# Kernel tuning notes

Measured on AMD Instinct MI355X. Metric: run time of the kernel, lower is better.

## Reference

```python
import jax, jax.numpy as jnp
import numpy as np

EMBED_DIM = 1024
NUM_HEADS = 16
HEAD_DIM = EMBED_DIM // NUM_HEADS


def setup_inputs() -> dict:
    key = jax.random.key(0)
    ks = jax.random.split(key, 9)
    B, S, E = 4, 2048, EMBED_DIM
    scale = 1.0 / np.sqrt(E)
    x = jax.random.normal(ks[0], (B, S, E), dtype=jnp.float32)
    # Linear layers: weight [E, E] (out, in) and bias [E], torch-style init scale
    Wq = jax.random.uniform(ks[1], (E, E), jnp.float32, -scale, scale)
    bq = jax.random.uniform(ks[2], (E,), jnp.float32, -scale, scale)
    Wk = jax.random.uniform(ks[3], (E, E), jnp.float32, -scale, scale)
    bk = jax.random.uniform(ks[4], (E,), jnp.float32, -scale, scale)
    Wv = jax.random.uniform(ks[5], (E, E), jnp.float32, -scale, scale)
    bv = jax.random.uniform(ks[6], (E,), jnp.float32, -scale, scale)
    Wo = jax.random.uniform(ks[7], (E, E), jnp.float32, -scale, scale)
    bo = jax.random.uniform(ks[8], (E,), jnp.float32, -scale, scale)
    return {"x": x, "Wq": Wq, "bq": bq, "Wk": Wk, "bk": bk,
            "Wv": Wv, "bv": bv, "Wo": Wo, "bo": bo}


def reference(x, Wq, bq, Wk, bk, Wv, bv, Wo, bo):
    B, S, E = x.shape
    H, D = NUM_HEADS, HEAD_DIM

    def proj(W, b):
        # torch Linear: x @ W.T + b ; reshape to [B, H, S, D]
        y = jnp.einsum('bse,fe->bsf', x, W) + b
        return y.reshape(B, S, H, D).transpose(0, 2, 1, 3)

    Q = proj(Wq, bq)
    K = proj(Wk, bk)
    V = proj(Wv, bv)
    scores = jnp.einsum('bhqd,bhkd->bhqk', Q, K) / jnp.sqrt(
        jnp.asarray(D, dtype=jnp.float32))
    attn = jax.nn.softmax(scores, axis=-1)
    out = jnp.einsum('bhqk,bhkd->bhqd', attn, V)
    out = out.transpose(0, 2, 1, 3).reshape(B, S, E)
    out = jnp.einsum('bse,fe->bsf', out, Wo) + bo
    return out
```

## Files before the change

### kernel.cpp

```cpp
#include <hip/hip_runtime.h>
#include <math.h>

#define SEQ 2048
#define EMB 1024
#define NH 16
#define HD 64
#define BATCH 4
#define MROWS (BATCH * SEQ)

typedef unsigned short u16;
typedef unsigned int u32;
typedef _Float16 f16;
using half8   = __attribute__((ext_vector_type(8))) f16;
using fp16x2  = __attribute__((ext_vector_type(2))) __fp16;
using vfloat4 = __attribute__((ext_vector_type(4))) float;

__device__ __forceinline__ u16 f2h(float f) {
    union { f16 h; u16 u; } x; x.h = (f16)f; return x.u;
}
__device__ __forceinline__ u32 pk2h(float a, float b) {
    union { fp16x2 h; u32 u; } x;
    x.h = __builtin_amdgcn_cvt_pkrtz(a, b);
    return x.u;
}
__device__ __forceinline__ float exp2v(float x) {
    float r; asm("v_exp_f32 %0, %1" : "=v"(r) : "v"(x)); return r;
}

__device__ __forceinline__ void gload16(const void* g, void* l) {
    __builtin_amdgcn_global_load_lds(
        (const __attribute__((address_space(1))) void*)g,
        (__attribute__((address_space(3))) void*)l, 16, 0, 0);
}

__global__ __launch_bounds__(256) void cvt_kernel(
    const float* __restrict__ in, u16* __restrict__ out, int n4)
{
    int idx = blockIdx.x * 256 + threadIdx.x;
    if (idx >= n4) return;
    float4 v = ((const float4*)in)[idx];
    u32 lo = pk2h(v.x, v.y);
    u32 hi = pk2h(v.z, v.w);
    ((uint2*)out)[idx] = make_uint2(lo, hi);
}

__global__ __launch_bounds__(256) void gemm_qkv_kernel(
    const u16* __restrict__ A, const u16* __restrict__ Wqkv,
    const float* __restrict__ bq, const float* __restrict__ bk,
    const float* __restrict__ bv,
    u16* __restrict__ Qo, u16* __restrict__ Ko, u16* __restrict__ Vo,
    float sq)
{
    __shared__ char lds[16384];
    char* As = lds;
    char* Bs = lds + 8192;
    const int tid = threadIdx.x, wave = tid >> 6, lane = tid & 63;
    const int bm = blockIdx.y, bn = blockIdx.x;
    const int mat = bn >> 3;
    const int wr = wave >> 1, wc = wave & 1;

    const int srow  = wave * 16 + (lane >> 2);
    const int sslot = lane & 3;
    const int ldso  = wave * 1024 + (lane << 4);
    const u16* Ab = A    + (size_t)bm * 128 * EMB;
    const u16* Wb = Wqkv + (size_t)bn * 128 * EMB;

    vfloat4 acc[4][4] = {};

    for (int k0 = 0; k0 < EMB; k0 += 32) {
        __syncthreads();
        #pragma unroll
        for (int i2 = 0; i2 < 2; ++i2) {
            int row = i2 * 64 + srow;
            int ko  = ((sslot ^ ((row >> 1) & 3)) << 3);
            gload16(Ab + (size_t)row * EMB + k0 + ko, As + i2 * 4096 + ldso);
            gload16(Wb + (size_t)row * EMB + k0 + ko, Bs + i2 * 4096 + ldso);
        }
        __syncthreads();

        half8 af[4], bfr[4];
        #pragma unroll
        for (int m = 0; m < 4; ++m) {
            int r = wr * 64 + m * 16 + (lane & 15);
            af[m] = *(const half8*)(As + r * 64 + ((((lane >> 4) ^ ((r >> 1) & 3)) << 4)));
        }
        #pragma unroll
        for (int n = 0; n < 4; ++n) {
            int r = wc * 64 + n * 16 + (lane & 15);
            bfr[n] = *(const half8*)(Bs + r * 64 + ((((lane >> 4) ^ ((r >> 1) & 3)) << 4)));
        }
        #pragma unroll
        for (int m = 0; m < 4; ++m)
            #pragma unroll
            for (int n = 0; n < 4; ++n)
                acc[m][n] = __builtin_amdgcn_mfma_f32_16x16x32_f16(af[m], bfr[n], acc[m][n], 0, 0, 0);
    }

    const float* bp = (mat == 0) ? bq : ((mat == 1) ? bk : bv);
    const float scale = (mat == 0) ? sq : 1.0f;
    u16* Co = (mat == 0) ? Qo : ((mat == 1) ? Ko : Vo);
    const int row0 = bm * 128 + wr * 64;
    const int col0 = (bn & 7) * 128 + wc * 64;

    #pragma unroll
    for (int n = 0; n < 4; ++n) {
        int col = col0 + n * 16 + (lane & 15);
        float bb = bp[col];
        int h = col >> 6, d = col & 63;
        #pragma unroll
        for (int m = 0; m < 4; ++m)
            #pragma unroll
            for (int j = 0; j < 4; ++j) {
                int row = row0 + m * 16 + (lane >> 4) * 4 + j;
                int b = row >> 11, s = row & (SEQ - 1);
                float val = (acc[m][n][j] + bb) * scale;
                if (mat != 2) {
                    Co[(((size_t)(b * NH + h)) * SEQ + s) * HD + d] = f2h(val);
                } else {
                    Co[(((size_t)(b * NH + h)) * HD + d) * SEQ + s] = f2h(val);
                }
            }
    }
}

__global__ __launch_bounds__(256) void gemm_f16_kernel(
    const u16* __restrict__ A, const u16* __restrict__ W,
    const float* __restrict__ bias, float* __restrict__ C)
{
    __shared__ char lds[16384];
    char* As = lds;
    char* Bs = lds + 8192;
    const int tid = threadIdx.x, wave = tid >> 6, lane = tid & 63;
    const int bm = blockIdx.y, bn = blockIdx.x;
    const int wr = wave >> 1, wc = wave & 1;

    const int srow  = wave * 16 + (lane >> 2);
    const int sslot = lane & 3;
    const int ldso  = wave * 1024 + (lane << 4);
    const u16* Ab = A + (size_t)bm * 128 * EMB;
    const u16* Wb = W + (size_t)bn * 128 * EMB;

    vfloat4 acc[4][4] = {};

    for (int k0 = 0; k0 < EMB; k0 += 32) {
        __syncthreads();
        #pragma unroll
        for (int i2 = 0; i2 < 2; ++i2) {
            int row = i2 * 64 + srow;
            int ko  = ((sslot ^ ((row >> 1) & 3)) << 3);
            gload16(Ab + (size_t)row * EMB + k0 + ko, As + i2 * 4096 + ldso);
            gload16(Wb + (size_t)row * EMB + k0 + ko, Bs + i2 * 4096 + ldso);
        }
        __syncthreads();

        half8 af[4], bfr[4];
        #pragma unroll
        for (int m = 0; m < 4; ++m) {
            int r = wr * 64 + m * 16 + (lane & 15);
            af[m] = *(const half8*)(As + r * 64 + ((((lane >> 4) ^ ((r >> 1) & 3)) << 4)));
        }
        #pragma unroll
        for (int n = 0; n < 4; ++n) {
            int r = wc * 64 + n * 16 + (lane & 15);
            bfr[n] = *(const half8*)(Bs + r * 64 + ((((lane >> 4) ^ ((r >> 1) & 3)) << 4)));
        }
        #pragma unroll
        for (int m = 0; m < 4; ++m)
            #pragma unroll
            for (int n = 0; n < 4; ++n)
                acc[m][n] = __builtin_amdgcn_mfma_f32_16x16x32_f16(af[m], bfr[n], acc[m][n], 0, 0, 0);
    }

    const int row0 = bm * 128 + wr * 64, col0 = bn * 128 + wc * 64;
    #pragma unroll
    for (int n = 0; n < 4; ++n) {
        int col = col0 + n * 16 + (lane & 15);
        float bb = bias[col];
        #pragma unroll
        for (int m = 0; m < 4; ++m)
            #pragma unroll
            for (int j = 0; j < 4; ++j) {
                int row = row0 + m * 16 + (lane >> 4) * 4 + j;
                C[(size_t)row * EMB + col] = acc[m][n][j] + bb;
            }
    }
}

__device__ __forceinline__ void stage_rows(const u16* g, int rstride, char* dst,
                                           int wave, int lane) {
    int r = wave * 8 + (lane >> 3), sl = lane & 7;
    #pragma unroll
    for (int i2 = 0; i2 < 2; ++i2) {
        int row = i2 * 32 + r;
        gload16(g + (size_t)row * rstride + ((sl ^ (row & 7)) << 3),
                dst + i2 * 4096 + wave * 1024 + (lane << 4));
    }
}

__global__ __launch_bounds__(256) void attn_kernel(
    const u16* __restrict__ Q, const u16* __restrict__ K,
    const u16* __restrict__ Vt, u16* __restrict__ O)
{
    __shared__ char lds[40960];
    char* QPs = lds;
    char* Kb0 = lds + 8192;
    char* Kb1 = lds + 16384;
    char* Vb0 = lds + 24576;
    char* Vb1 = lds + 32768;

    const int tid = threadIdx.x, wave = tid >> 6, lane = tid & 63;
    const int c = lane >> 4, li = lane & 15;
    const int bh = blockIdx.y;
    const int q0 = blockIdx.x << 6;

    const u16* Qg = Q  + ((size_t)bh * SEQ + q0) * HD;
    const u16* Kg = K  + (size_t)bh * SEQ * HD;
    const u16* Vg = Vt + (size_t)bh * HD * SEQ;

    stage_rows(Qg, HD, QPs, wave, lane);
    stage_rows(Kg, HD, Kb0, wave, lane);
    stage_rows(Vg, SEQ, Vb0, wave, lane);
    __syncthreads();

    half8 qf[2];
    {
        int q = wave * 16 + li;
        #pragma unroll
        for (int cc = 0; cc < 2; ++cc)
            qf[cc] = *(const half8*)(QPs + q * 128 + (((4 * cc + c) ^ (q & 7)) << 4));
    }

    const half8 ones8 = {1, 1, 1, 1, 1, 1, 1, 1};
    char* Pw = QPs + wave * 2048;
    vfloat4 o[4] = {};
    vfloat4 o5 = {};
    float m_ = -1e30f;

    for (int kt = 0; kt < SEQ / 64; ++kt) {
        char* Kc = (kt & 1) ? Kb1 : Kb0;
        char* Vc = (kt & 1) ? Vb1 : Vb0;
        if (kt < SEQ / 64 - 1) {
            stage_rows(Kg + (size_t)(kt + 1) * 64 * HD, HD,
                       (kt & 1) ? Kb0 : Kb1, wave, lane);
            stage_rows(Vg + (kt + 1) * 64, SEQ,
                       (kt & 1) ? Vb0 : Vb1, wave, lane);
        }

        vfloat4 st[4] = {};
        #pragma unroll
        for (int n = 0; n < 4; ++n) {
            int key = 16 * n + li;
            #pragma unroll
            for (int cc = 0; cc < 2; ++cc) {
                half8 kb = *(const half8*)(Kc + key * 128 + (((4 * cc + c) ^ (li & 7)) << 4));
                st[n] = __builtin_amdgcn_mfma_f32_16x16x32_f16(kb, qf[cc], st[n], 0, 0, 0);
            }
        }

        float t0 = fmaxf(fmaxf(st[0][0], st[0][1]), fmaxf(st[0][2], st[0][3]));
        float t1 = fmaxf(fmaxf(st[1][0], st[1][1]), fmaxf(st[1][2], st[1][3]));
        float t2 = fmaxf(fmaxf(st[2][0], st[2][1]), fmaxf(st[2][2], st[2][3]));
        float t3 = fmaxf(fmaxf(st[3][0], st[3][1]), fmaxf(st[3][2], st[3][3]));
        float pm = fmaxf(fmaxf(t0, t1), fmaxf(t2, t3));
        pm = fmaxf(pm, __shfl_xor(pm, 16));
        pm = fmaxf(pm, __shfl_xor(pm, 32));

        if (__any(pm > m_ + 8.0f)) {
            float mn = fmaxf(m_, pm);
            float al = exp2v(m_ - mn);
            m_ = mn;
            o5 = o5 * al;
            #pragma unroll
            for (int n = 0; n < 4; ++n) o[n] = o[n] * al;
        }

        #pragma unroll
        for (int n = 0; n < 4; ++n)
            #pragma unroll
            for (int j = 0; j < 4; ++j)
                st[n][j] = exp2v(st[n][j] - m_);

        #pragma unroll
        for (int n = 0; n < 4; ++n) {
            u32 w0 = pk2h(st[n][0], st[n][1]);
            u32 w1 = pk2h(st[n][2], st[n][3]);
            *(uint2*)(Pw + li * 128 + (((2 * n + (c >> 1)) ^ (li & 7)) << 4) + ((c & 1) << 3))
                = make_uint2(w0, w1);
        }

        half8 pf[2];
        #pragma unroll
        for (int cc = 0; cc < 2; ++cc)
            pf[cc] = *(const half8*)(Pw + li * 128 + (((4 * cc + c) ^ (li & 7)) << 4));

        #pragma unroll
        for (int n = 0; n < 4; ++n) {
            int r = 16 * n + li;
            #pragma unroll
            for (int cc = 0; cc < 2; ++cc) {
                half8 vf = *(const half8*)(Vc + r * 128 + (((4 * cc + c) ^ (li & 7)) << 4));
                o[n] = __builtin_amdgcn_mfma_f32_16x16x32_f16(vf, pf[cc], o[n], 0, 0, 0);
            }
        }
        #pragma unroll
        for (int cc = 0; cc < 2; ++cc)
            o5 = __builtin_amdgcn_mfma_f32_16x16x32_f16(ones8, pf[cc], o5, 0, 0, 0);

        __syncthreads();
    }

    const int b = bh >> 4, h = bh & 15;
    const int sg = q0 + wave * 16 + li;
    const size_t rowo = ((size_t)b * SEQ + sg) * EMB + h * 64;
    float inv = 1.0f / o5[0];
    #pragma unroll
    for (int n = 0; n < 4; ++n) {
        u32 w0 = pk2h(o[n][0] * inv, o[n][1] * inv);
        u32 w1 = pk2h(o[n][2] * inv, o[n][3] * inv);
        *(uint2*)(O + rowo + 16 * n + 4 * c) = make_uint2(w0, w1);
    }
}

extern "C" void kernel_launch(void* const* d_in, const int* in_sizes, int n_in,
                              void* d_out, int out_size, void* d_ws, size_t ws_size,
                              hipStream_t stream) {
    const float* x  = (const float*)d_in[0];
    const float* Wq = (const float*)d_in[1];
    const float* bq = (const float*)d_in[2];
    const float* Wk = (const float*)d_in[3];
    const float* bk = (const float*)d_in[4];
    const float* Wv = (const float*)d_in[5];
    const float* bv = (const float*)d_in[6];
    const float* Wo = (const float*)d_in[7];
    const float* bo = (const float*)d_in[8];
    float* out = (float*)d_out;

    char* ws = (char*)d_ws;
    u16* xh   = (u16*)(ws);
    u16* Qh   = (u16*)(ws + ((size_t)16 << 20));
    u16* Kh   = (u16*)(ws + ((size_t)32 << 20));
    u16* Vh   = (u16*)(ws + ((size_t)48 << 20));
    u16* Ah   = (u16*)(ws + ((size_t)64 << 20));
    u16* Wqkv = (u16*)(ws + ((size_t)80 << 20));
    u16* Woh  = (u16*)(ws + ((size_t)88 << 20));

    const int nX4 = (MROWS * EMB) / 4;
    const int nW4 = (EMB * EMB) / 4;

    cvt_kernel<<<(nX4 + 255) / 256, 256, 0, stream>>>(x, xh, nX4);
    cvt_kernel<<<(nW4 + 255) / 256, 256, 0, stream>>>(Wq, Wqkv, nW4);
    cvt_kernel<<<(nW4 + 255) / 256, 256, 0, stream>>>(Wk, Wqkv + (size_t)EMB * EMB, nW4);
    cvt_kernel<<<(nW4 + 255) / 256, 256, 0, stream>>>(Wv, Wqkv + (size_t)2 * EMB * EMB, nW4);
    cvt_kernel<<<(nW4 + 255) / 256, 256, 0, stream>>>(Wo, Woh, nW4);

    const float SCALE_Q = 0.125f * 1.4426950408889634f;
    gemm_qkv_kernel<<<dim3(3 * EMB / 128, MROWS / 128), 256, 0, stream>>>(
        xh, Wqkv, bq, bk, bv, Qh, Kh, Vh, SCALE_Q);

    attn_kernel<<<dim3(SEQ / 64, BATCH * NH), 256, 0, stream>>>(Qh, Kh, Vh, Ah);

    gemm_f16_kernel<<<dim3(EMB / 128, MROWS / 128), 256, 0, stream>>>(Ah, Woh, bo, out);
}
```

Measured before the change: 265.4 us.

## Process two query tiles per attention block and merge conversion kernels

The attention kernel now handles 128 query rows per block, with each wave keeping two 16-row query fragments. This reuses every staged K/V tile for twice the queries, halving K/V global traffic and the block count. The five fp32-to-fp16 conversion launches are merged into one kernel to cut launch overhead. The cost is higher register pressure and fewer blocks (1024 vs 2048), which may lower occupancy.

```diff
diff --git a/kernel.cpp b/kernel.cpp
--- a/kernel.cpp
+++ b/kernel.cpp
@@ -33,15 +33,27 @@
         (__attribute__((address_space(3))) void*)l, 16, 0, 0);
 }
 
-__global__ __launch_bounds__(256) void cvt_kernel(
-    const float* __restrict__ in, u16* __restrict__ out, int n4)
+__global__ __launch_bounds__(256) void cvt5_kernel(
+    const float* __restrict__ x,  const float* __restrict__ wq,
+    const float* __restrict__ wk, const float* __restrict__ wv,
+    const float* __restrict__ wo,
+    uint2* __restrict__ xh, uint2* __restrict__ wqkv, uint2* __restrict__ woh)
 {
-    int idx = blockIdx.x * 256 + threadIdx.x;
-    if (idx >= n4) return;
-    float4 v = ((const float4*)in)[idx];
-    u32 lo = pk2h(v.x, v.y);
-    u32 hi = pk2h(v.z, v.w);
-    ((uint2*)out)[idx] = make_uint2(lo, hi);
+    int gid = blockIdx.x * 256 + threadIdx.x;
+    const float4* src; uint2* dst; int o;
+    if (gid < (1 << 21)) {
+        src = (const float4*)x; dst = xh; o = gid;
+    } else {
+        int g = gid - (1 << 21);
+        int r = g >> 18;
+        o = g & ((1 << 18) - 1);
+        if      (r == 0) { src = (const float4*)wq; dst = wqkv; }
+        else if (r == 1) { src = (const float4*)wk; dst = wqkv + (1 << 18); }
+        else if (r == 2) { src = (const float4*)wv; dst = wqkv + (2 << 18); }
+        else             { src = (const float4*)wo; dst = woh; }
+    }
+    float4 v = src[o];
+    dst[o] = make_uint2(pk2h(v.x, v.y), pk2h(v.z, v.w));
 }
 
 __global__ __launch_bounds__(256) void gemm_qkv_kernel(
@@ -211,7 +223,7 @@
     const int tid = threadIdx.x, wave = tid >> 6, lane = tid & 63;
     const int c = lane >> 4, li = lane & 15;
     const int bh = blockIdx.y;
-    const int q0 = blockIdx.x << 6;
+    const int q0 = blockIdx.x << 7;
 
     const u16* Qg = Q  + ((size_t)bh * SEQ + q0) * HD;
     const u16* Kg = K  + (size_t)bh * SEQ * HD;
@@ -222,19 +234,23 @@
     stage_rows(Vg, SEQ, Vb0, wave, lane);
     __syncthreads();
 
-    half8 qf[2];
-    {
-        int q = wave * 16 + li;
-        #pragma unroll
-        for (int cc = 0; cc < 2; ++cc)
-            qf[cc] = *(const half8*)(QPs + q * 128 + (((4 * cc + c) ^ (q & 7)) << 4));
-    }
+    half8 qf[2][2];
+    const int q = wave * 16 + li;
+    #pragma unroll
+    for (int cc = 0; cc < 2; ++cc)
+        qf[0][cc] = *(const half8*)(QPs + q * 128 + (((4 * cc + c) ^ (q & 7)) << 4));
+    __syncthreads();
+    stage_rows(Qg + (size_t)64 * HD, HD, QPs, wave, lane);
+    __syncthreads();
+    #pragma unroll
+    for (int cc = 0; cc < 2; ++cc)
+        qf[1][cc] = *(const half8*)(QPs + q * 128 + (((4 * cc + c) ^ (q & 7)) << 4));
 
     const half8 ones8 = {1, 1, 1, 1, 1, 1, 1, 1};
     char* Pw = QPs + wave * 2048;
-    vfloat4 o[4] = {};
-    vfloat4 o5 = {};
-    float m_ = -1e30f;
+    vfloat4 o0[4] = {}, o1[4] = {};
+    vfloat4 l0 = {}, l1 = {};
+    float m0 = -1e30f, m1 = -1e30f;
 
     for (int kt = 0; kt < SEQ / 64; ++kt) {
         char* Kc = (kt & 1) ? Kb1 : Kb0;
@@ -246,52 +262,78 @@
                        (kt & 1) ? Vb0 : Vb1, wave, lane);
         }
 
-        vfloat4 st[4] = {};
+        vfloat4 s0[4] = {}, s1[4] = {};
         #pragma unroll
         for (int n = 0; n < 4; ++n) {
             int key = 16 * n + li;
             #pragma unroll
             for (int cc = 0; cc < 2; ++cc) {
                 half8 kb = *(const half8*)(Kc + key * 128 + (((4 * cc + c) ^ (li & 7)) << 4));
-                st[n] = __builtin_amdgcn_mfma_f32_16x16x32_f16(kb, qf[cc], st[n], 0, 0, 0);
+                s0[n] = __builtin_amdgcn_mfma_f32_16x16x32_f16(kb, qf[0][cc], s0[n], 0, 0, 0);
+                s1[n] = __builtin_amdgcn_mfma_f32_16x16x32_f16(kb, qf[1][cc], s1[n], 0, 0, 0);
             }
         }
 
-        float t0 = fmaxf(fmaxf(st[0][0], st[0][1]), fmaxf(st[0][2], st[0][3]));
-        float t1 = fmaxf(fmaxf(st[1][0], st[1][1]), fmaxf(st[1][2], st[1][3]));
-        float t2 = fmaxf(fmaxf(st[2][0], st[2][1]), fmaxf(st[2][2], st[2][3]));
-        float t3 = fmaxf(fmaxf(st[3][0], st[3][1]), fmaxf(st[3][2], st[3][3]));
-        float pm = fmaxf(fmaxf(t0, t1), fmaxf(t2, t3));
-        pm = fmaxf(pm, __shfl_xor(pm, 16));
-        pm = fmaxf(pm, __shfl_xor(pm, 32));
-
-        if (__any(pm > m_ + 8.0f)) {
-            float mn = fmaxf(m_, pm);
-            float al = exp2v(m_ - mn);
-            m_ = mn;
-            o5 = o5 * al;
-            #pragma unroll
-            for (int n = 0; n < 4; ++n) o[n] = o[n] * al;
+        float pm0, pm1;
+        {
+            float a = fmaxf(fmaxf(s0[0][0], s0[0][1]), fmaxf(s0[0][2], s0[0][3]));
+            float b = fmaxf(fmaxf(s0[1][0], s0[1][1]), fmaxf(s0[1][2], s0[1][3]));
+            float d = fmaxf(fmaxf(s0[2][0], s0[2][1]), fmaxf(s0[2][2], s0[2][3]));
+            float e = fmaxf(fmaxf(s0[3][0], s0[3][1]), fmaxf(s0[3][2], s0[3][3]));
+            pm0 = fmaxf(fmaxf(a, b), fmaxf(d, e));
+            a = fmaxf(fmaxf(s1[0][0], s1[0][1]), fmaxf(s1[0][2], s1[0][3]));
+            b = fmaxf(fmaxf(s1[1][0], s1[1][1]), fmaxf(s1[1][2], s1[1][3]));
+            d = fmaxf(fmaxf(s1[2][0], s1[2][1]), fmaxf(s1[2][2], s1[2][3]));
+            e = fmaxf(fmaxf(s1[3][0], s1[3][1]), fmaxf(s1[3][2], s1[3][3]));
+            pm1 = fmaxf(fmaxf(a, b), fmaxf(d, e));
+        }
+        pm0 = fmaxf(pm0, __shfl_xor(pm0, 16));
+        pm0 = fmaxf(pm0, __shfl_xor(pm0, 32));
+        pm1 = fmaxf(pm1, __shfl_xor(pm1, 16));
+        pm1 = fmaxf(pm1, __shfl_xor(pm1, 32));
+
+        if (__any(fmaxf(pm0 - m0, pm1 - m1) > 8.0f)) {
+            float mn = fmaxf(m0, pm0);
+            float al = exp2v(m0 - mn);
+            m0 = mn; l0 = l0 * al;
+            #pragma unroll
+            for (int n = 0; n < 4; ++n) o0[n] = o0[n] * al;
+            mn = fmaxf(m1, pm1);
+            al = exp2v(m1 - mn);
+            m1 = mn; l1 = l1 * al;
+            #pragma unroll
+            for (int n = 0; n < 4; ++n) o1[n] = o1[n] * al;
         }
 
         #pragma unroll
         for (int n = 0; n < 4; ++n)
             #pragma unroll
-            for (int j = 0; j < 4; ++j)
-                st[n][j] = exp2v(st[n][j] - m_);
-
-        #pragma unroll
-        for (int n = 0; n < 4; ++n) {
-            u32 w0 = pk2h(st[n][0], st[n][1]);
-            u32 w1 = pk2h(st[n][2], st[n][3]);
+            for (int j = 0; j < 4; ++j) {
+                s0[n][j] = exp2v(s0[n][j] - m0);
+                s1[n][j] = exp2v(s1[n][j] - m1);
+            }
+
+        half8 pf0[2], pf1[2];
+        #pragma unroll
+        for (int n = 0; n < 4; ++n) {
+            u32 w0 = pk2h(s0[n][0], s0[n][1]);
+            u32 w1 = pk2h(s0[n][2], s0[n][3]);
             *(uint2*)(Pw + li * 128 + (((2 * n + (c >> 1)) ^ (li & 7)) << 4) + ((c & 1) << 3))
                 = make_uint2(w0, w1);
         }
-
-        half8 pf[2];
         #pragma unroll
         for (int cc = 0; cc < 2; ++cc)
-            pf[cc] = *(const half8*)(Pw + li * 128 + (((4 * cc + c) ^ (li & 7)) << 4));
+            pf0[cc] = *(const half8*)(Pw + li * 128 + (((4 * cc + c) ^ (li & 7)) << 4));
+        #pragma unroll
+        for (int n = 0; n < 4; ++n) {
+            u32 w0 = pk2h(s1[n][0], s1[n][1]);
+            u32 w1 = pk2h(s1[n][2], s1[n][3]);
+            *(uint2*)(Pw + li * 128 + (((2 * n + (c >> 1)) ^ (li & 7)) << 4) + ((c & 1) << 3))
+                = make_uint2(w0, w1);
+        }
+        #pragma unroll
+        for (int cc = 0; cc < 2; ++cc)
+            pf1[cc] = *(const half8*)(Pw + li * 128 + (((4 * cc + c) ^ (li & 7)) << 4));
 
         #pragma unroll
         for (int n = 0; n < 4; ++n) {
@@ -299,25 +341,32 @@
             #pragma unroll
             for (int cc = 0; cc < 2; ++cc) {
                 half8 vf = *(const half8*)(Vc + r * 128 + (((4 * cc + c) ^ (li & 7)) << 4));
-                o[n] = __builtin_amdgcn_mfma_f32_16x16x32_f16(vf, pf[cc], o[n], 0, 0, 0);
+                o0[n] = __builtin_amdgcn_mfma_f32_16x16x32_f16(vf, pf0[cc], o0[n], 0, 0, 0);
+                o1[n] = __builtin_amdgcn_mfma_f32_16x16x32_f16(vf, pf1[cc], o1[n], 0, 0, 0);
             }
         }
         #pragma unroll
-        for (int cc = 0; cc < 2; ++cc)
-            o5 = __builtin_amdgcn_mfma_f32_16x16x32_f16(ones8, pf[cc], o5, 0, 0, 0);
+        for (int cc = 0; cc < 2; ++cc) {
+            l0 = __builtin_amdgcn_mfma_f32_16x16x32_f16(ones8, pf0[cc], l0, 0, 0, 0);
+            l1 = __builtin_amdgcn_mfma_f32_16x16x32_f16(ones8, pf1[cc], l1, 0, 0, 0);
+        }
 
         __syncthreads();
     }
 
     const int b = bh >> 4, h = bh & 15;
-    const int sg = q0 + wave * 16 + li;
-    const size_t rowo = ((size_t)b * SEQ + sg) * EMB + h * 64;
-    float inv = 1.0f / o5[0];
+    const size_t r0 = ((size_t)b * SEQ + q0 + wave * 16 + li) * EMB + h * 64;
+    const size_t r1 = ((size_t)b * SEQ + q0 + 64 + wave * 16 + li) * EMB + h * 64;
+    float i0 = 1.0f / l0[0];
+    float i1 = 1.0f / l1[0];
     #pragma unroll
     for (int n = 0; n < 4; ++n) {
-        u32 w0 = pk2h(o[n][0] * inv, o[n][1] * inv);
-        u32 w1 = pk2h(o[n][2] * inv, o[n][3] * inv);
-        *(uint2*)(O + rowo + 16 * n + 4 * c) = make_uint2(w0, w1);
+        *(uint2*)(O + r0 + 16 * n + 4 * c) =
+            make_uint2(pk2h(o0[n][0] * i0, o0[n][1] * i0),
+                       pk2h(o0[n][2] * i0, o0[n][3] * i0));
+        *(uint2*)(O + r1 + 16 * n + 4 * c) =
+            make_uint2(pk2h(o1[n][0] * i1, o1[n][1] * i1),
+                       pk2h(o1[n][2] * i1, o1[n][3] * i1));
     }
 }
 
@@ -344,20 +393,16 @@
     u16* Wqkv = (u16*)(ws + ((size_t)80 << 20));
     u16* Woh  = (u16*)(ws + ((size_t)88 << 20));
 
-    const int nX4 = (MROWS * EMB) / 4;
-    const int nW4 = (EMB * EMB) / 4;
-
-    cvt_kernel<<<(nX4 + 255) / 256, 256, 0, stream>>>(x, xh, nX4);
-    cvt_kernel<<<(nW4 + 255) / 256, 256, 0, stream>>>(Wq, Wqkv, nW4);
-    cvt_kernel<<<(nW4 + 255) / 256, 256, 0, stream>>>(Wk, Wqkv + (size_t)EMB * EMB, nW4);
-    cvt_kernel<<<(nW4 + 255) / 256, 256, 0, stream>>>(Wv, Wqkv + (size_t)2 * EMB * EMB, nW4);
-    cvt_kernel<<<(nW4 + 255) / 256, 256, 0, stream>>>(Wo, Woh, nW4);
+    const int nCvt = (1 << 21) + (1 << 20);
+
+    cvt5_kernel<<<nCvt / 256, 256, 0, stream>>>(
+        x, Wq, Wk, Wv, Wo, (uint2*)xh, (uint2*)Wqkv, (uint2*)Woh);
 
     const float SCALE_Q = 0.125f * 1.4426950408889634f;
     gemm_qkv_kernel<<<dim3(3 * EMB / 128, MROWS / 128), 256, 0, stream>>>(
         xh, Wqkv, bq, bk, bv, Qh, Kh, Vh, SCALE_Q);
 
-    attn_kernel<<<dim3(SEQ / 64, BATCH * NH), 256, 0, stream>>>(Qh, Kh, Vh, Ah);
+    attn_kernel<<<dim3(SEQ / 128, BATCH * NH), 256, 0, stream>>>(Qh, Kh, Vh, Ah);
 
     gemm_f16_kernel<<<dim3(EMB / 128, MROWS / 128), 256, 0, stream>>>(Ah, Woh, bo, out);
 }
```

Measured after the change: 247.1 us. 1.07x faster.
